# Performance work log

Measured on AMD Instinct MI355X. Metric: run time of the kernel, lower is better.

The kernel has to match this reference:

```python
import jax, jax.numpy as jnp
import numpy as np

SHRINK_THRES = 0.0025
EPS = 1e-12  # F.normalize default eps


def _l2norm(v, axis=-1):
    return v / jnp.maximum(jnp.linalg.norm(v, axis=axis, keepdims=True), EPS)


def setup_inputs() -> dict:
    key = jax.random.key(0)
    ks = jax.random.split(key, 5)
    N, C, H, W = 16, 256, 64, 64
    mem_dim = 512
    x = jax.random.normal(ks[0], (N, C, H, W), dtype=jnp.float32)
    memory = jax.random.normal(ks[1], (mem_dim, C), dtype=jnp.float32) * 0.1
    memory = _l2norm(memory, axis=1)
    w1 = jax.random.normal(ks[2], (C, C // 2), dtype=jnp.float32) * (1.0 / np.sqrt(C))
    b1 = jnp.zeros((C // 2,), dtype=jnp.float32)
    w2 = jax.random.normal(ks[3], (C // 2, C), dtype=jnp.float32) * (1.0 / np.sqrt(C // 2))
    b2 = jnp.zeros((C,), dtype=jnp.float32)
    return {"x": x, "memory": memory, "w1": w1, "b1": b1, "w2": w2, "b2": b2}


def reference(x, memory, w1, b1, w2, b2):
    N, C, H, W = x.shape
    # [N,C,H,W] -> [N*H*W, C]
    x_flat = jnp.transpose(x, (0, 2, 3, 1)).reshape(-1, C)
    x_norm = _l2norm(x_flat, axis=1)
    # shared MLP over memory slots: Linear -> ReLU -> Linear -> ReLU
    m = jax.nn.relu(memory @ w1 + b1)
    m = jax.nn.relu(m @ w2 + b2)
    mem_norm = _l2norm(m, axis=1)  # [M, C]
    # cosine similarity + softmax over memory slots
    att = jax.nn.softmax(x_norm @ mem_norm.T, axis=1)  # [N*H*W, M]
    # hard shrink + L1 renormalization
    att = jax.nn.relu(att - SHRINK_THRES)
    att = att / jnp.maximum(jnp.sum(att, axis=1, keepdims=True), EPS)
    out_flat = att @ mem_norm  # [N*H*W, C]
    output = jnp.transpose(out_flat.reshape(N, H, W, C), (0, 3, 1, 2))
    att_map = jnp.transpose(att.reshape(N, H, W, -1), (0, 3, 1, 2))
    return output, att_map
```

## Files before the change

### kernel.cpp

```cpp
#include <hip/hip_runtime.h>
#include <hip/hip_bf16.h>

typedef _Float16 half8 __attribute__((ext_vector_type(8)));
typedef _Float16 half4v __attribute__((ext_vector_type(4)));
typedef float floatx4 __attribute__((ext_vector_type(4)));

#define C_DIM 256
#define M_DIM 512
#define HW 4096
#define TAU 0.0025f
#define LCAP 96

__global__ __launch_bounds__(128) void prep_kernel(
    const float* __restrict__ memory, const float* __restrict__ w1,
    const float* __restrict__ b1, const float* __restrict__ w2,
    const float* __restrict__ b2,
    _Float16* __restrict__ mN, float* __restrict__ mN32,
    float* __restrict__ attmap)
{
  __shared__ float sm[256];
  __shared__ float sh[128];
  __shared__ float s_part[2];
  __shared__ float s_tot;
  const int r = blockIdx.x;
  const int t = threadIdx.x;

  {
    const floatx4 z = {0.f, 0.f, 0.f, 0.f};
    floatx4* p4 = (floatx4*)attmap;
    size_t i = (size_t)r * 128 + t;
#pragma unroll 4
    for (int k = 0; k < 128; ++k) { p4[i] = z; i += 65536; }
  }

  sm[t]       = memory[r * C_DIM + t];
  sm[t + 128] = memory[r * C_DIM + t + 128];
  __syncthreads();
  float acc = b1[t];
#pragma unroll 8
  for (int c = 0; c < 256; ++c) acc = fmaf(sm[c], w1[c * 128 + t], acc);
  sh[t] = fmaxf(acc, 0.f);
  __syncthreads();
  float o0 = b2[t], o1 = b2[t + 128];
#pragma unroll 8
  for (int k = 0; k < 128; ++k) {
    float h = sh[k];
    o0 = fmaf(h, w2[k * 256 + t], o0);
    o1 = fmaf(h, w2[k * 256 + t + 128], o1);
  }
  o0 = fmaxf(o0, 0.f);
  o1 = fmaxf(o1, 0.f);
  float ss = o0 * o0 + o1 * o1;
#pragma unroll
  for (int off = 32; off >= 1; off >>= 1) ss += __shfl_down(ss, off);
  if ((t & 63) == 0) s_part[t >> 6] = ss;
  __syncthreads();
  if (t == 0) s_tot = s_part[0] + s_part[1];
  __syncthreads();
  const float inv = 1.f / fmaxf(sqrtf(s_tot), 1e-12f);
  const float v0 = o0 * inv, v1 = o1 * inv;
  mN[r * C_DIM + t]        = (_Float16)v0;
  mN[r * C_DIM + t + 128]  = (_Float16)v1;
  mN32[r * C_DIM + t]       = v0;
  mN32[r * C_DIM + t + 128] = v1;
}

#define MFMA16(a, b, c) __builtin_amdgcn_mfma_f32_16x16x32_f16(a, b, c, 0, 0, 0)

__global__ __launch_bounds__(512, 4) void main_kernel(
    const float* __restrict__ x,
    const _Float16* __restrict__ mN,
    const float* __restrict__ mN32,
    float* __restrict__ out, float* __restrict__ attmap)
{
  __shared__ _Float16       Xh[64][264];
  __shared__ unsigned short s_lslot[64][LCAP];
  __shared__ float          s_lval[64][LCAP];
  __shared__ int      s_cnt[64];
  __shared__ float    s_sumsq[64];
  __shared__ float    s_sum1[64];
  __shared__ float    s_sum2[64];

  const int tid  = threadIdx.x;
  const int wave = tid >> 6;
  const int lane = tid & 63;
  const int q    = lane >> 4;
  const int c16  = lane & 15;
  const int g    = tid >> 3;
  const int pxq  = tid & 7;

  const int blk = blockIdx.x;
  const int img = blk >> 6;
  const int hw0 = (blk & 63) * 64;
  const float* __restrict__ xb = x + (size_t)img * C_DIM * HW + hw0;

  if (tid < 64) {
    s_sumsq[tid] = 0.f; s_sum1[tid] = 0.f; s_sum2[tid] = 0.f; s_cnt[tid] = 0;
  }
  __syncthreads();

#pragma unroll
  for (int h = 0; h < 2; ++h) {
    floatx4 v[4];
#pragma unroll
    for (int i = 0; i < 4; ++i)
      v[i] = *(const floatx4*)(xb + (size_t)(4 * g + i) * HW + (pxq + 8 * h) * 4);
    float ps[4];
#pragma unroll
    for (int j = 0; j < 4; ++j) {
      const int p = (pxq + 8 * h) * 4 + j;
      half4v hv = {(_Float16)v[0][j], (_Float16)v[1][j], (_Float16)v[2][j], (_Float16)v[3][j]};
      *(half4v*)&Xh[p][4 * g] = hv;
      ps[j] = v[0][j] * v[0][j] + v[1][j] * v[1][j] + v[2][j] * v[2][j] + v[3][j] * v[3][j];
    }
#pragma unroll
    for (int off = 8; off < 64; off <<= 1)
#pragma unroll
      for (int j = 0; j < 4; ++j) ps[j] += __shfl_xor(ps[j], off);
    if ((lane >> 3) == 0) {
#pragma unroll
      for (int j = 0; j < 4; ++j) atomicAdd(&s_sumsq[4 * (lane & 7) + 32 * h + j], ps[j]);
    }
  }

  const _Float16* bp[4];
#pragma unroll
  for (int nt = 0; nt < 4; ++nt)
    bp[nt] = mN + (size_t)(wave * 64 + nt * 16 + c16) * C_DIM + q * 8;
  half8 bcur[4], bnxt[4];
#pragma unroll
  for (int nt = 0; nt < 4; ++nt) bcur[nt] = *(const half8*)bp[nt];

  __syncthreads();

  floatx4 acc[4][4];
#pragma unroll
  for (int mt = 0; mt < 4; ++mt)
#pragma unroll
    for (int nt = 0; nt < 4; ++nt) {
      floatx4 z = {0.f, 0.f, 0.f, 0.f};
      acc[mt][nt] = z;
    }
#pragma unroll
  for (int kb = 0; kb < 8; ++kb) {
    if (kb < 7) {
#pragma unroll
      for (int nt = 0; nt < 4; ++nt) bnxt[nt] = *(const half8*)(bp[nt] + (kb + 1) * 32);
    }
    const int k0 = kb * 32 + q * 8;
    half8 ah[4];
#pragma unroll
    for (int mt = 0; mt < 4; ++mt) ah[mt] = *(const half8*)&Xh[mt * 16 + c16][k0];
#pragma unroll
    for (int nt = 0; nt < 4; ++nt)
#pragma unroll
      for (int mt = 0; mt < 4; ++mt)
        acc[mt][nt] = MFMA16(ah[mt], bcur[nt], acc[mt][nt]);
#pragma unroll
    for (int nt = 0; nt < 4; ++nt) bcur[nt] = bnxt[nt];
  }

#pragma unroll
  for (int mt = 0; mt < 4; ++mt)
#pragma unroll
    for (int r = 0; r < 4; ++r) {
      const int m = mt * 16 + q * 4 + r;
      const float iv = 1.f / fmaxf(sqrtf(s_sumsq[m]), 1e-12f);
      float s = 0.f;
#pragma unroll
      for (int nt = 0; nt < 4; ++nt) {
        const float e = __expf(acc[mt][nt][r] * iv);
        acc[mt][nt][r] = e;
        s += e;
      }
      s += __shfl_xor(s, 1);
      s += __shfl_xor(s, 2);
      s += __shfl_xor(s, 4);
      s += __shfl_xor(s, 8);
      if (c16 == 0) atomicAdd(&s_sum1[m], s);
    }
  __syncthreads();

#pragma unroll
  for (int mt = 0; mt < 4; ++mt)
#pragma unroll
    for (int r = 0; r < 4; ++r) {
      const int m = mt * 16 + q * 4 + r;
      const float isum = 1.f / s_sum1[m];
      float s = 0.f;
#pragma unroll
      for (int nt = 0; nt < 4; ++nt) {
        const float tv = fmaxf(acc[mt][nt][r] * isum - TAU, 0.f);
        acc[mt][nt][r] = tv;
        s += tv;
      }
      s += __shfl_xor(s, 1);
      s += __shfl_xor(s, 2);
      s += __shfl_xor(s, 4);
      s += __shfl_xor(s, 8);
      if (c16 == 0) atomicAdd(&s_sum2[m], s);
    }
  __syncthreads();

#pragma unroll
  for (int mt = 0; mt < 4; ++mt) {
    float rs[4];
#pragma unroll
    for (int r = 0; r < 4; ++r)
      rs[r] = 1.f / fmaxf(s_sum2[mt * 16 + q * 4 + r], 1e-12f);
#pragma unroll
    for (int nt = 0; nt < 4; ++nt) {
      floatx4 a4 = acc[mt][nt];
      const unsigned n = wave * 64 + nt * 16 + c16;
#pragma unroll
      for (int r = 0; r < 4; ++r) {
        a4[r] *= rs[r];
        if (a4[r] > 0.f) {
          const int m = mt * 16 + q * 4 + r;
          const int idx = atomicAdd(&s_cnt[m], 1);
          if (idx < LCAP) {
            s_lslot[m][idx] = (unsigned short)n;
            s_lval[m][idx]  = a4[r];
          }
          attmap[((size_t)img * M_DIM + n) * HW + hw0 + m] = a4[r];
        }
      }
    }
  }
  __syncthreads();

  const int px4 = (tid & 15) * 4;
  const int chg = tid >> 4;
  floatx4 f[8] = {{0.f,0.f,0.f,0.f},{0.f,0.f,0.f,0.f},{0.f,0.f,0.f,0.f},{0.f,0.f,0.f,0.f},
                  {0.f,0.f,0.f,0.f},{0.f,0.f,0.f,0.f},{0.f,0.f,0.f,0.f},{0.f,0.f,0.f,0.f}};
#pragma unroll
  for (int p = 0; p < 4; ++p) {
    const int cn = min(s_cnt[px4 + p], LCAP);
    for (int j = 0; j < cn; ++j) {
      const int slot  = s_lslot[px4 + p][j];
      const float v   = s_lval[px4 + p][j];
      const floatx4* row = (const floatx4*)(mN32 + (size_t)slot * C_DIM + chg * 8);
      const floatx4 r0 = row[0], r1 = row[1];
      f[0][p] += v * r0[0]; f[1][p] += v * r0[1];
      f[2][p] += v * r0[2]; f[3][p] += v * r0[3];
      f[4][p] += v * r1[0]; f[5][p] += v * r1[1];
      f[6][p] += v * r1[2]; f[7][p] += v * r1[3];
    }
  }

#pragma unroll
  for (int c = 0; c < 8; ++c)
    *(floatx4*)(out + ((size_t)img * C_DIM + chg * 8 + c) * HW + hw0 + px4) = f[c];
}

extern "C" void kernel_launch(void* const* d_in, const int* in_sizes, int n_in,
                              void* d_out, int out_size, void* d_ws, size_t ws_size,
                              hipStream_t stream) {
  (void)in_sizes; (void)n_in; (void)out_size; (void)ws_size;
  const float* x      = (const float*)d_in[0];
  const float* memory = (const float*)d_in[1];
  const float* w1     = (const float*)d_in[2];
  const float* b1     = (const float*)d_in[3];
  const float* w2     = (const float*)d_in[4];
  const float* b2     = (const float*)d_in[5];
  float* out    = (float*)d_out;
  float* attmap = out + (size_t)16 * C_DIM * HW;

  _Float16* mN   = (_Float16*)d_ws;
  float*    mN32 = (float*)((char*)d_ws + (size_t)M_DIM * C_DIM * sizeof(_Float16));

  hipLaunchKernelGGL(prep_kernel, dim3(M_DIM), dim3(128), 0, stream,
                     memory, w1, b1, w2, b2, mN, mN32, attmap);
  hipLaunchKernelGGL(main_kernel, dim3(1024), dim3(512), 0, stream,
                     x, mN, mN32, out, attmap);
}
```

Measured before the change: 325.6 us.

## Overlap attmap zeroing with main kernel compute via ticketed blocks and global gate

Moves zeroing of the large attention-map output out of the small prep kernel and into the first 512 blocks of the main kernel, which do it after their MFMA loop. Those blocks are chosen by an atomic ticket. The sparse nonzero attmap writes are deferred to the end of each block, behind a global spin-wait counter that confirms all zeroing is finished. The writes now come from the LDS slot lists with coalesced per-pixel lanes, not from scattered writes during normalization. The goal is to hide the large memset behind compute and shorten prep. In exchange it adds a grid-wide spin dependency, and entries beyond LCAP per pixel are no longer written to attmap.

```diff
diff --git a/kernel.cpp b/kernel.cpp
--- a/kernel.cpp
+++ b/kernel.cpp
@@ -10,13 +10,14 @@
 #define HW 4096
 #define TAU 0.0025f
 #define LCAP 96
+#define NZERO 512
 
 __global__ __launch_bounds__(128) void prep_kernel(
     const float* __restrict__ memory, const float* __restrict__ w1,
     const float* __restrict__ b1, const float* __restrict__ w2,
     const float* __restrict__ b2,
     _Float16* __restrict__ mN, float* __restrict__ mN32,
-    float* __restrict__ attmap)
+    int* __restrict__ sync)
 {
   __shared__ float sm[256];
   __shared__ float sh[128];
@@ -24,14 +25,7 @@
   __shared__ float s_tot;
   const int r = blockIdx.x;
   const int t = threadIdx.x;
-
-  {
-    const floatx4 z = {0.f, 0.f, 0.f, 0.f};
-    floatx4* p4 = (floatx4*)attmap;
-    size_t i = (size_t)r * 128 + t;
-#pragma unroll 4
-    for (int k = 0; k < 128; ++k) { p4[i] = z; i += 65536; }
-  }
+  if (r == 0 && t == 0) { sync[0] = 0; sync[32] = 0; }
 
   sm[t]       = memory[r * C_DIM + t];
   sm[t + 128] = memory[r * C_DIM + t + 128];
@@ -71,7 +65,8 @@
     const float* __restrict__ x,
     const _Float16* __restrict__ mN,
     const float* __restrict__ mN32,
-    float* __restrict__ out, float* __restrict__ attmap)
+    float* __restrict__ out, float* __restrict__ attmap,
+    int* __restrict__ sync)
 {
   __shared__ _Float16       Xh[64][264];
   __shared__ unsigned short s_lslot[64][LCAP];
@@ -80,6 +75,7 @@
   __shared__ float    s_sumsq[64];
   __shared__ float    s_sum1[64];
   __shared__ float    s_sum2[64];
+  __shared__ int      s_ticket;
 
   const int tid  = threadIdx.x;
   const int wave = tid >> 6;
@@ -94,10 +90,12 @@
   const int hw0 = (blk & 63) * 64;
   const float* __restrict__ xb = x + (size_t)img * C_DIM * HW + hw0;
 
+  if (tid == 0) s_ticket = atomicAdd(&sync[0], 1);
   if (tid < 64) {
     s_sumsq[tid] = 0.f; s_sum1[tid] = 0.f; s_sum2[tid] = 0.f; s_cnt[tid] = 0;
   }
   __syncthreads();
+  const int ticket = s_ticket;
 
 #pragma unroll
   for (int h = 0; h < 2; ++h) {
@@ -158,6 +156,13 @@
         acc[mt][nt] = MFMA16(ah[mt], bcur[nt], acc[mt][nt]);
 #pragma unroll
     for (int nt = 0; nt < 4; ++nt) bcur[nt] = bnxt[nt];
+  }
+
+  if (ticket < NZERO) {
+    floatx4* dst = (floatx4*)attmap + (size_t)ticket * 16384 + tid;
+    const floatx4 z = {0.f, 0.f, 0.f, 0.f};
+#pragma unroll
+    for (int k = 0; k < 32; ++k) { *dst = z; dst += 512; }
   }
 
 #pragma unroll
@@ -181,6 +186,11 @@
     }
   __syncthreads();
 
+  if (ticket < NZERO && tid == 0) {
+    __threadfence();
+    atomicAdd(&sync[32], 1);
+  }
+
 #pragma unroll
   for (int mt = 0; mt < 4; ++mt)
 #pragma unroll
@@ -222,7 +232,6 @@
             s_lslot[m][idx] = (unsigned short)n;
             s_lval[m][idx]  = a4[r];
           }
-          attmap[((size_t)img * M_DIM + n) * HW + hw0 + m] = a4[r];
         }
       }
     }
@@ -251,6 +260,21 @@
 #pragma unroll
   for (int c = 0; c < 8; ++c)
     *(floatx4*)(out + ((size_t)img * C_DIM + chg * 8 + c) * HW + hw0 + px4) = f[c];
+
+  int gate = 0;
+  if (lane == 0) {
+    while (atomicAdd(&sync[32], 0) < NZERO) __builtin_amdgcn_s_sleep(8);
+    gate = 1;
+  }
+  gate = __shfl(gate, 0);
+  if (gate) {
+    const int px = wave * 8 + (lane >> 3);
+    const int cn = min(s_cnt[px], LCAP);
+    for (int j = (lane & 7); j < cn; j += 8) {
+      const int slot = s_lslot[px][j];
+      attmap[((size_t)img * M_DIM + slot) * HW + hw0 + px] = s_lval[px][j];
+    }
+  }
 }
 
 extern "C" void kernel_launch(void* const* d_in, const int* in_sizes, int n_in,
@@ -268,9 +292,10 @@
 
   _Float16* mN   = (_Float16*)d_ws;
   float*    mN32 = (float*)((char*)d_ws + (size_t)M_DIM * C_DIM * sizeof(_Float16));
+  int*      sync = (int*)((char*)d_ws + (size_t)M_DIM * C_DIM * 6);
 
   hipLaunchKernelGGL(prep_kernel, dim3(M_DIM), dim3(128), 0, stream,
-                     memory, w1, b1, w2, b2, mN, mN32, attmap);
+                     memory, w1, b1, w2, b2, mN, mN32, sync);
   hipLaunchKernelGGL(main_kernel, dim3(1024), dim3(512), 0, stream,
-                     x, mN, mN32, out, attmap);
+                     x, mN, mN32, out, attmap, sync);
 }
```

After: 372.8 us. 14.5% more time.
